# Kernel optimization log

Measured on AMD Instinct MI355X. Metric: run time of the kernel, lower is better.

The kernel has to match this reference:

```python
import jax, jax.numpy as jnp
import numpy as np

N_NODES = 100000
N_EDGES = 3200000
HID = 16


def _graph_conv(x, src, dst, w_rel, w_root, b_rel, num_nodes):
    # PyG GraphConv: out_i = lin_rel(sum_{j in N(i)} x_j) + lin_root(x_i)
    agg = jax.ops.segment_sum(x[src], dst, num_segments=num_nodes)  # [N, d_in]
    return agg @ w_rel + b_rel + x @ w_root


def setup_inputs() -> dict:
    key = jax.random.key(0)
    ks = jax.random.split(key, 8)
    x = jax.random.normal(ks[0], (N_NODES, 1), dtype=jnp.float32)
    edge_index = jax.random.randint(ks[1], (2, N_EDGES), 0, N_NODES, dtype=jnp.int64)
    s = 1.0 / np.sqrt(HID)
    return {
        "x": x,
        "edge_index": edge_index,
        "enc_w_rel": jax.random.uniform(ks[2], (1, HID), jnp.float32, -1.0, 1.0),
        "enc_w_root": jax.random.uniform(ks[3], (1, HID), jnp.float32, -1.0, 1.0),
        "enc_b": jnp.zeros((HID,), jnp.float32),
        "proc_w_rel": jax.random.uniform(ks[4], (HID, HID), jnp.float32, -s, s),
        "proc_w_root": jax.random.uniform(ks[5], (HID, HID), jnp.float32, -s, s),
        "proc_b": jnp.zeros((HID,), jnp.float32),
        "dec_w_rel": jax.random.uniform(ks[6], (HID, 1), jnp.float32, -s, s),
        "dec_w_root": jax.random.uniform(ks[7], (HID, 1), jnp.float32, -s, s),
        "dec_b": jnp.zeros((1,), jnp.float32),
    }


def reference(x, edge_index, enc_w_rel, enc_w_root, enc_b,
              proc_w_rel, proc_w_root, proc_b,
              dec_w_rel, dec_w_root, dec_b):
    num_nodes = x.shape[0]
    src, dst = edge_index[0], edge_index[1]
    z = _graph_conv(x, src, dst, enc_w_rel, enc_w_root, enc_b, num_nodes)
    z = jax.nn.relu(z)
    z = _graph_conv(z, src, dst, proc_w_rel, proc_w_root, proc_b, num_nodes)
    y = _graph_conv(z, src, dst, dec_w_rel, dec_w_root, dec_b, num_nodes)
    return jax.nn.relu(y)
```

## Files before the change

### kernel.cpp

```cpp
#include <hip/hip_runtime.h>
#include <hip/hip_bf16.h>

#define HID 16
#define SB_BITS 11
#define SBLK (1 << SB_BITS)
#define SUBS 128
#define NBMAX 64
#define GSTRIDE 16
#define PT_THREADS 512
#define PT_K 8
#define PT_EDGES (PT_THREADS * PT_K)
#define ROWP 65

__global__ void k_init(int* __restrict__ p, int n) {
    int i = blockIdx.x * blockDim.x + threadIdx.x;
    if (i < n) p[i] = 0;
}

__global__ void __launch_bounds__(PT_THREADS)
k_passA(const int* __restrict__ src, const int* __restrict__ dst,
        unsigned* __restrict__ bucketsA, int* __restrict__ gcurA,
        int E, int nb, int capA) {
    __shared__ int cnt[NBMAX];
    __shared__ int pos[NBMAX];
    __shared__ int gbase[NBMAX];
    __shared__ unsigned reorder[PT_EDGES];
    __shared__ unsigned char bbk[PT_EDGES];
    int tb = blockIdx.x * PT_EDGES;
    int nE = min(PT_EDGES, E - tb);
    if (threadIdx.x < nb) cnt[threadIdx.x] = 0;
    __syncthreads();
    int kk[PT_K]; int rk[PT_K]; unsigned pk[PT_K];
    int ebase = tb + threadIdx.x * PT_K;
    if (ebase + PT_K <= E) {
        uint4 s0 = *(const uint4*)(src + ebase);
        uint4 s1 = *(const uint4*)(src + ebase + 4);
        uint4 d0 = *(const uint4*)(dst + ebase);
        uint4 d1 = *(const uint4*)(dst + ebase + 4);
        int ss[PT_K] = {(int)s0.x,(int)s0.y,(int)s0.z,(int)s0.w,
                        (int)s1.x,(int)s1.y,(int)s1.z,(int)s1.w};
        int dd[PT_K] = {(int)d0.x,(int)d0.y,(int)d0.z,(int)d0.w,
                        (int)d1.x,(int)d1.y,(int)d1.z,(int)d1.w};
#pragma unroll
        for (int k = 0; k < PT_K; k++) {
            int b = dd[k] >> SB_BITS;
            kk[k] = b;
            pk[k] = ((unsigned)(dd[k] & (SBLK - 1)) << 17) | (unsigned)ss[k];
            rk[k] = atomicAdd(&cnt[b], 1);
        }
    } else {
#pragma unroll
        for (int k = 0; k < PT_K; k++) {
            int e = ebase + k;
            if (e < E) {
                int s = src[e], d = dst[e];
                int b = d >> SB_BITS;
                kk[k] = b;
                pk[k] = ((unsigned)(d & (SBLK - 1)) << 17) | (unsigned)s;
                rk[k] = atomicAdd(&cnt[b], 1);
            } else kk[k] = -1;
        }
    }
    __syncthreads();
    if (threadIdx.x == 0) {
        int acc = 0;
        for (int b = 0; b < nb; b++) { pos[b] = acc; acc += cnt[b]; }
    }
    __syncthreads();
    if (threadIdx.x < nb && cnt[threadIdx.x] > 0)
        gbase[threadIdx.x] = atomicAdd(&gcurA[threadIdx.x * GSTRIDE], cnt[threadIdx.x]);
    __syncthreads();
#pragma unroll
    for (int k = 0; k < PT_K; k++) {
        if (kk[k] >= 0) {
            int idx = pos[kk[k]] + rk[k];
            reorder[idx] = pk[k];
            bbk[idx] = (unsigned char)kk[k];
        }
    }
    __syncthreads();
    for (int idx = threadIdx.x; idx < nE; idx += PT_THREADS) {
        int b = bbk[idx];
        int g = gbase[b] + (idx - pos[b]);
        if (g < capA) bucketsA[(size_t)b * capA + g] = reorder[idx];
    }
}

__global__ void __launch_bounds__(PT_THREADS)
k_passB(const unsigned* __restrict__ bucketsA, const int* __restrict__ gcurA,
        unsigned* __restrict__ bucketsB, int* __restrict__ gcurB,
        int capA, int capSub, int tilesB) {
    int j = blockIdx.x / tilesB;
    int tile = blockIdx.x - j * tilesB;
    int cnt_j = min(gcurA[j * GSTRIDE], capA);
    int tb = tile * PT_EDGES;
    if (tb >= cnt_j) return;
    int nE = min(PT_EDGES, cnt_j - tb);
    __shared__ int cnt[SUBS];
    __shared__ int pos[SUBS];
    __shared__ int gb[SUBS];
    __shared__ unsigned reorder[PT_EDGES];
    if (threadIdx.x < SUBS) cnt[threadIdx.x] = 0;
    __syncthreads();
    const unsigned* in = bucketsA + (size_t)j * capA + tb;
    int kk[PT_K]; int rk[PT_K]; unsigned pk[PT_K];
    int ebase = threadIdx.x * PT_K;
    if (ebase + PT_K <= nE) {
        uint4 p0 = *(const uint4*)(in + ebase);
        uint4 p1 = *(const uint4*)(in + ebase + 4);
        unsigned pp[PT_K] = {p0.x, p0.y, p0.z, p0.w, p1.x, p1.y, p1.z, p1.w};
#pragma unroll
        for (int k = 0; k < PT_K; k++) {
            int s = (int)(pp[k] >> 21);
            kk[k] = s;
            pk[k] = pp[k];
            rk[k] = atomicAdd(&cnt[s], 1);
        }
    } else {
#pragma unroll
        for (int k = 0; k < PT_K; k++) {
            int e = ebase + k;
            if (e < nE) {
                unsigned p = in[e];
                int s = (int)(p >> 21);
                kk[k] = s;
                pk[k] = p;
                rk[k] = atomicAdd(&cnt[s], 1);
            } else kk[k] = -1;
        }
    }
    __syncthreads();
    if (threadIdx.x == 0) {
        int acc = 0;
        for (int s = 0; s < SUBS; s++) { pos[s] = acc; acc += cnt[s]; }
    }
    __syncthreads();
    if (threadIdx.x < SUBS && cnt[threadIdx.x] > 0)
        gb[threadIdx.x] = atomicAdd(&gcurB[j * SUBS + threadIdx.x], cnt[threadIdx.x]);
    __syncthreads();
#pragma unroll
    for (int k = 0; k < PT_K; k++) {
        if (kk[k] >= 0) {
            int idx = pos[kk[k]] + rk[k];
            reorder[idx] = pk[k];
        }
    }
    __syncthreads();
    for (int idx = threadIdx.x; idx < nE; idx += PT_THREADS) {
        unsigned p = reorder[idx];
        int s = (int)(p >> 21);
        unsigned outp = ((p & 0x1FFFFu) << 4) | ((p >> 17) & 15u);
        int g = gb[s] + (idx - pos[s]);
        if (g < capSub) bucketsB[(size_t)(j * SUBS + s) * capSub + g] = outp;
    }
}

__global__ void __launch_bounds__(256)
k_agg1enc(const unsigned* __restrict__ bk2, const int* __restrict__ gcurB,
          const float* __restrict__ x,
          const float* __restrict__ ewrel, const float* __restrict__ ewroot,
          const float* __restrict__ eb,
          const float* __restrict__ pwrel, const float* __restrict__ pwroot,
          const float* __restrict__ dwrel, const float* __restrict__ dwroot,
          float* __restrict__ SAB, float* __restrict__ G1, float* __restrict__ G2,
          int capSub, int N) {
    __shared__ float P[4 * 16 * ROWP];
    __shared__ float su1[HID], su2[HID], sv1[HID], sv2[HID];
    __shared__ float swr[HID], swo[HID], sbb[HID];
    int t = threadIdx.x;
    if (t < 64) {
        int k = t & 15, w = t >> 4;
        const float* M  = (w < 2) ? pwrel : pwroot;
        const float* vv = ((w & 1) == 0) ? dwrel : dwroot;
        float acc = 0.f;
        for (int h = 0; h < HID; h++) acc += M[k * HID + h] * vv[h];
        if (w == 0) su1[k] = acc;
        else if (w == 1) su2[k] = acc;
        else if (w == 2) sv1[k] = acc;
        else sv2[k] = acc;
    }
    if (t < HID) { swr[t] = ewrel[t]; swo[t] = ewroot[t]; sbb[t] = eb[t]; }
    int wv = t >> 6, lane = t & 63;
    int q = blockIdx.x * 4 + wv;
    float* p = P + wv * 16 * ROWP;
#pragma unroll
    for (int d = 0; d < 16; d++) p[d * ROWP + lane] = 0.f;
    __syncthreads();
    int cnt = min(gcurB[q], capSub);
    const unsigned* bk = bk2 + (size_t)q * capSub;
    int base = 0;
    for (; base + 256 <= cnt; base += 256) {
        uint4 p4 = *(const uint4*)(bk + base + (lane << 2));
        float v0 = x[p4.x >> 4], v1 = x[p4.y >> 4], v2 = x[p4.z >> 4], v3 = x[p4.w >> 4];
        p[(int)(p4.x & 15) * ROWP + lane] += v0;
        p[(int)(p4.y & 15) * ROWP + lane] += v1;
        p[(int)(p4.z & 15) * ROWP + lane] += v2;
        p[(int)(p4.w & 15) * ROWP + lane] += v3;
    }
    for (int e = base + lane; e < cnt; e += 64) {
        unsigned pk = bk[e];
        p[(int)(pk & 15) * ROWP + lane] += x[pk >> 4];
    }
    __builtin_amdgcn_wave_barrier();
    int d = lane & 15, c0 = (lane >> 4) * 16;
    float s = 0.f;
#pragma unroll
    for (int k = 0; k < 16; k++) s += p[d * ROWP + c0 + k];
    s += __shfl_xor(s, 16);
    s += __shfl_xor(s, 32);
    if (lane < 16) {
        int n = q * 16 + lane;
        if (n < N) {
            float a1 = s, xi = x[n];
            float sa = 0.f, sb = 0.f, g1 = 0.f, g2 = 0.f;
#pragma unroll
            for (int h = 0; h < HID; h++) {
                float z = fmaxf(fmaf(a1, swr[h], fmaf(xi, swo[h], sbb[h])), 0.f);
                sa = fmaf(z, su1[h], sa);
                sb = fmaf(z, su2[h], sb);
                g1 = fmaf(z, sv1[h], g1);
                g2 = fmaf(z, sv2[h], g2);
            }
            ((float2*)SAB)[n] = make_float2(sa, sb);
            G1[n] = g1; G2[n] = g2;
        }
    }
}

__global__ void __launch_bounds__(256)
k_agg2mid(const unsigned* __restrict__ bk2, const int* __restrict__ gcurB,
          const float* __restrict__ SAB,
          const float* __restrict__ G1, const float* __restrict__ G2,
          const float* __restrict__ pb, const float* __restrict__ dwrel,
          const float* __restrict__ dwroot, const float* __restrict__ db,
          float* __restrict__ BETA, float* __restrict__ R,
          int capSub, int N) {
    __shared__ float2 P2[4 * 16 * ROWP];
    __shared__ float sc1, sc2, sbd;
    int t = threadIdx.x;
    if (t == 0) {
        float c1 = 0.f, c2 = 0.f;
        for (int h = 0; h < HID; h++) { c1 += pb[h] * dwrel[h]; c2 += pb[h] * dwroot[h]; }
        sc1 = c1; sc2 = c2; sbd = db[0];
    }
    int wv = t >> 6, lane = t & 63;
    int q = blockIdx.x * 4 + wv;
    float2* pw = P2 + wv * 16 * ROWP;
#pragma unroll
    for (int d = 0; d < 16; d++) pw[d * ROWP + lane] = make_float2(0.f, 0.f);
    __syncthreads();
    int cnt = min(gcurB[q], capSub);
    const unsigned* bk = bk2 + (size_t)q * capSub;
    const float2* v2 = (const float2*)SAB;
    int base = 0;
    for (; base + 256 <= cnt; base += 256) {
        uint4 p4 = *(const uint4*)(bk + base + (lane << 2));
        float2 v0 = v2[p4.x >> 4], v1 = v2[p4.y >> 4];
        float2 w2 = v2[p4.z >> 4], w3 = v2[p4.w >> 4];
        float2* s0 = &pw[(int)(p4.x & 15) * ROWP + lane];
        s0->x += v0.x; s0->y += v0.y;
        float2* s1 = &pw[(int)(p4.y & 15) * ROWP + lane];
        s1->x += v1.x; s1->y += v1.y;
        float2* s2 = &pw[(int)(p4.z & 15) * ROWP + lane];
        s2->x += w2.x; s2->y += w2.y;
        float2* s3 = &pw[(int)(p4.w & 15) * ROWP + lane];
        s3->x += w3.x; s3->y += w3.y;
    }
    for (int e = base + lane; e < cnt; e += 64) {
        unsigned pk = bk[e];
        float2 v = v2[pk >> 4];
        float2* s = &pw[(int)(pk & 15) * ROWP + lane];
        s->x += v.x; s->y += v.y;
    }
    __builtin_amdgcn_wave_barrier();
    int d = lane & 15, c0 = (lane >> 4) * 16;
    float sa = 0.f, sb = 0.f;
#pragma unroll
    for (int k = 0; k < 16; k++) {
        float2 v = pw[d * ROWP + c0 + k];
        sa += v.x; sb += v.y;
    }
    sa += __shfl_xor(sa, 16); sa += __shfl_xor(sa, 32);
    sb += __shfl_xor(sb, 16); sb += __shfl_xor(sb, 32);
    if (lane < 16) {
        int n = q * 16 + lane;
        if (n < N) {
            BETA[n] = sa + G1[n] + sc1;
            R[n]    = sb + G2[n] + sc2 + sbd;
        }
    }
}

__global__ void __launch_bounds__(256)
k_agg1f(const unsigned* __restrict__ bk2, const int* __restrict__ gcurB,
        const float* __restrict__ val, const float* __restrict__ R,
        float* __restrict__ out, int capSub, int N) {
    __shared__ float P[4 * 16 * ROWP];
    int wv = threadIdx.x >> 6, lane = threadIdx.x & 63;
    int q = blockIdx.x * 4 + wv;
    float* p = P + wv * 16 * ROWP;
#pragma unroll
    for (int d = 0; d < 16; d++) p[d * ROWP + lane] = 0.f;
    int cnt = min(gcurB[q], capSub);
    const unsigned* bk = bk2 + (size_t)q * capSub;
    int base = 0;
    for (; base + 256 <= cnt; base += 256) {
        uint4 p4 = *(const uint4*)(bk + base + (lane << 2));
        float v0 = val[p4.x >> 4], v1 = val[p4.y >> 4];
        float v2 = val[p4.z >> 4], v3 = val[p4.w >> 4];
        p[(int)(p4.x & 15) * ROWP + lane] += v0;
        p[(int)(p4.y & 15) * ROWP + lane] += v1;
        p[(int)(p4.z & 15) * ROWP + lane] += v2;
        p[(int)(p4.w & 15) * ROWP + lane] += v3;
    }
    for (int e = base + lane; e < cnt; e += 64) {
        unsigned pk = bk[e];
        p[(int)(pk & 15) * ROWP + lane] += val[pk >> 4];
    }
    __builtin_amdgcn_wave_barrier();
    int d = lane & 15, c0 = (lane >> 4) * 16;
    float s = 0.f;
#pragma unroll
    for (int k = 0; k < 16; k++) s += p[d * ROWP + c0 + k];
    s += __shfl_xor(s, 16);
    s += __shfl_xor(s, 32);
    if (lane < 16) {
        int n = q * 16 + lane;
        if (n < N) out[n] = fmaxf(s + R[n], 0.f);
    }
}

extern "C" void kernel_launch(void* const* d_in, const int* in_sizes, int n_in,
                              void* d_out, int out_size, void* d_ws, size_t ws_size,
                              hipStream_t stream) {
    const float* x      = (const float*)d_in[0];
    const int*   ei     = (const int*)d_in[1];
    const float* ewrel  = (const float*)d_in[2];
    const float* ewroot = (const float*)d_in[3];
    const float* eb     = (const float*)d_in[4];
    const float* pwrel  = (const float*)d_in[5];
    const float* pwroot = (const float*)d_in[6];
    const float* pb     = (const float*)d_in[7];
    const float* dwrel  = (const float*)d_in[8];
    const float* dwroot = (const float*)d_in[9];
    const float* db     = (const float*)d_in[10];
    float* out = (float*)d_out;

    const int N = in_sizes[0];
    const int E = in_sizes[1] / 2;
    const int* src = ei;
    const int* dst = ei + E;

    const int nb = (N + SBLK - 1) >> SB_BITS;
    int capA = ((E / nb + 2048) + PT_EDGES - 1) & ~(PT_EDGES - 1);
    const int tilesB = capA / PT_EDGES;
    const int nq = nb * SUBS;
    int capSub = ((E / nq + 226) + 3) & ~3;

    size_t off = 0;
    int* gcurA = (int*)d_ws;                    off += NBMAX * GSTRIDE;
    int* gcurB = (int*)d_ws + off;              off += nq;
    const int zeroWords = (int)off;
    off = (off + 255) & ~(size_t)255;
    unsigned* bucketsA = (unsigned*)d_ws + off; off += (size_t)nb * capA;
    unsigned* bucketsB = (unsigned*)d_ws + off; off += (size_t)nq * capSub;
    float* SAB  = (float*)d_ws + off;           off += (size_t)2 * N;
    float* G1   = (float*)d_ws + off;           off += N;
    float* G2   = (float*)d_ws + off;           off += N;
    float* BETA = (float*)d_ws + off;           off += N;
    float* R    = (float*)d_ws + off;           off += N;

    const int ntilesA = (E + PT_EDGES - 1) / PT_EDGES;
    const int aggBlocks = nq / 4;

    hipLaunchKernelGGL(k_init, dim3((zeroWords + 255) / 256), dim3(256), 0, stream,
                       gcurA, zeroWords);
    hipLaunchKernelGGL(k_passA, dim3(ntilesA), dim3(PT_THREADS), 0, stream,
                       src, dst, bucketsA, gcurA, E, nb, capA);
    hipLaunchKernelGGL(k_passB, dim3(nb * tilesB), dim3(PT_THREADS), 0, stream,
                       bucketsA, gcurA, bucketsB, gcurB, capA, capSub, tilesB);

    hipLaunchKernelGGL(k_agg1enc, dim3(aggBlocks), dim3(256), 0, stream,
                       bucketsB, gcurB, x, ewrel, ewroot, eb, pwrel, pwroot,
                       dwrel, dwroot, SAB, G1, G2, capSub, N);
    hipLaunchKernelGGL(k_agg2mid, dim3(aggBlocks), dim3(256), 0, stream,
                       bucketsB, gcurB, SAB, G1, G2, pb, dwrel, dwroot, db,
                       BETA, R, capSub, N);
    hipLaunchKernelGGL(k_agg1f, dim3(aggBlocks), dim3(256), 0, stream,
                       bucketsB, gcurB, BETA, R, out, capSub, N);
}
```

Measured before the change: 174.2 us.

## Drop second bucketing pass; aggregate via LDS float atomics per coarse bucket

Removes the passB sub-bucket sort and its bucketsB buffer. Each aggregation now reads the coarse passA buckets directly, accumulates into a 2048-entry shared-memory array with float atomics, and flushes to global per-node accumulators with global atomics. Per-node epilogue math moves into separate elementwise kernels. This saves one full scatter of the edge list but adds LDS atomic contention, global atomics from many tiles per bucket, and extra kernel launches, and the result becomes order-nondeterministic.

```diff
diff --git a/kernel.cpp b/kernel.cpp
--- a/kernel.cpp
+++ b/kernel.cpp
@@ -1,16 +1,13 @@
 #include <hip/hip_runtime.h>
-#include <hip/hip_bf16.h>
 
 #define HID 16
 #define SB_BITS 11
 #define SBLK (1 << SB_BITS)
-#define SUBS 128
 #define NBMAX 64
 #define GSTRIDE 16
 #define PT_THREADS 512
 #define PT_K 8
 #define PT_EDGES (PT_THREADS * PT_K)
-#define ROWP 65
 
 __global__ void k_init(int* __restrict__ p, int n) {
     int i = blockIdx.x * blockDim.x + threadIdx.x;
@@ -87,84 +84,111 @@
 }
 
 __global__ void __launch_bounds__(PT_THREADS)
-k_passB(const unsigned* __restrict__ bucketsA, const int* __restrict__ gcurA,
-        unsigned* __restrict__ bucketsB, int* __restrict__ gcurB,
-        int capA, int capSub, int tilesB) {
-    int j = blockIdx.x / tilesB;
-    int tile = blockIdx.x - j * tilesB;
+k_aggA1(const unsigned* __restrict__ bucketsA, const int* __restrict__ gcurA,
+        const float* __restrict__ val, float* __restrict__ AGG,
+        int capA, int tilesA, int N) {
+    int j = blockIdx.x / tilesA;
+    int tile = blockIdx.x - j * tilesA;
     int cnt_j = min(gcurA[j * GSTRIDE], capA);
     int tb = tile * PT_EDGES;
     if (tb >= cnt_j) return;
     int nE = min(PT_EDGES, cnt_j - tb);
-    __shared__ int cnt[SUBS];
-    __shared__ int pos[SUBS];
-    __shared__ int gb[SUBS];
-    __shared__ unsigned reorder[PT_EDGES];
-    if (threadIdx.x < SUBS) cnt[threadIdx.x] = 0;
+    __shared__ float acc[SBLK];
+    for (int i = threadIdx.x; i < SBLK; i += PT_THREADS) acc[i] = 0.f;
     __syncthreads();
     const unsigned* in = bucketsA + (size_t)j * capA + tb;
-    int kk[PT_K]; int rk[PT_K]; unsigned pk[PT_K];
     int ebase = threadIdx.x * PT_K;
     if (ebase + PT_K <= nE) {
         uint4 p0 = *(const uint4*)(in + ebase);
         uint4 p1 = *(const uint4*)(in + ebase + 4);
         unsigned pp[PT_K] = {p0.x, p0.y, p0.z, p0.w, p1.x, p1.y, p1.z, p1.w};
-#pragma unroll
-        for (int k = 0; k < PT_K; k++) {
-            int s = (int)(pp[k] >> 21);
-            kk[k] = s;
-            pk[k] = pp[k];
-            rk[k] = atomicAdd(&cnt[s], 1);
-        }
+        float v[PT_K];
+#pragma unroll
+        for (int k = 0; k < PT_K; k++) v[k] = val[pp[k] & 0x1FFFFu];
+#pragma unroll
+        for (int k = 0; k < PT_K; k++) atomicAdd(&acc[pp[k] >> 17], v[k]);
     } else {
 #pragma unroll
         for (int k = 0; k < PT_K; k++) {
             int e = ebase + k;
             if (e < nE) {
                 unsigned p = in[e];
-                int s = (int)(p >> 21);
-                kk[k] = s;
-                pk[k] = p;
-                rk[k] = atomicAdd(&cnt[s], 1);
-            } else kk[k] = -1;
-        }
-    }
-    __syncthreads();
-    if (threadIdx.x == 0) {
-        int acc = 0;
-        for (int s = 0; s < SUBS; s++) { pos[s] = acc; acc += cnt[s]; }
-    }
-    __syncthreads();
-    if (threadIdx.x < SUBS && cnt[threadIdx.x] > 0)
-        gb[threadIdx.x] = atomicAdd(&gcurB[j * SUBS + threadIdx.x], cnt[threadIdx.x]);
-    __syncthreads();
-#pragma unroll
-    for (int k = 0; k < PT_K; k++) {
-        if (kk[k] >= 0) {
-            int idx = pos[kk[k]] + rk[k];
-            reorder[idx] = pk[k];
-        }
-    }
-    __syncthreads();
-    for (int idx = threadIdx.x; idx < nE; idx += PT_THREADS) {
-        unsigned p = reorder[idx];
-        int s = (int)(p >> 21);
-        unsigned outp = ((p & 0x1FFFFu) << 4) | ((p >> 17) & 15u);
-        int g = gb[s] + (idx - pos[s]);
-        if (g < capSub) bucketsB[(size_t)(j * SUBS + s) * capSub + g] = outp;
+                atomicAdd(&acc[p >> 17], val[p & 0x1FFFFu]);
+            }
+        }
+    }
+    __syncthreads();
+    int base_n = j << SB_BITS;
+    for (int i = threadIdx.x; i < SBLK; i += PT_THREADS) {
+        float v = acc[i];
+        int n = base_n + i;
+        if (n < N && v != 0.f) atomicAdd(&AGG[n], v);
+    }
+}
+
+__global__ void __launch_bounds__(PT_THREADS)
+k_aggA2(const unsigned* __restrict__ bucketsA, const int* __restrict__ gcurA,
+        const float* __restrict__ SAB, float* __restrict__ AGG2,
+        int capA, int tilesA, int N) {
+    int j = blockIdx.x / tilesA;
+    int tile = blockIdx.x - j * tilesA;
+    int cnt_j = min(gcurA[j * GSTRIDE], capA);
+    int tb = tile * PT_EDGES;
+    if (tb >= cnt_j) return;
+    int nE = min(PT_EDGES, cnt_j - tb);
+    __shared__ float accx[SBLK];
+    __shared__ float accy[SBLK];
+    for (int i = threadIdx.x; i < SBLK; i += PT_THREADS) { accx[i] = 0.f; accy[i] = 0.f; }
+    __syncthreads();
+    const unsigned* in = bucketsA + (size_t)j * capA + tb;
+    const float2* v2 = (const float2*)SAB;
+    int ebase = threadIdx.x * PT_K;
+    if (ebase + PT_K <= nE) {
+        uint4 p0 = *(const uint4*)(in + ebase);
+        uint4 p1 = *(const uint4*)(in + ebase + 4);
+        unsigned pp[PT_K] = {p0.x, p0.y, p0.z, p0.w, p1.x, p1.y, p1.z, p1.w};
+        float2 v[PT_K];
+#pragma unroll
+        for (int k = 0; k < PT_K; k++) v[k] = v2[pp[k] & 0x1FFFFu];
+#pragma unroll
+        for (int k = 0; k < PT_K; k++) {
+            int d = (int)(pp[k] >> 17);
+            atomicAdd(&accx[d], v[k].x);
+            atomicAdd(&accy[d], v[k].y);
+        }
+    } else {
+#pragma unroll
+        for (int k = 0; k < PT_K; k++) {
+            int e = ebase + k;
+            if (e < nE) {
+                unsigned p = in[e];
+                float2 v = v2[p & 0x1FFFFu];
+                int d = (int)(p >> 17);
+                atomicAdd(&accx[d], v.x);
+                atomicAdd(&accy[d], v.y);
+            }
+        }
+    }
+    __syncthreads();
+    int base_n = j << SB_BITS;
+    for (int i = threadIdx.x; i < SBLK; i += PT_THREADS) {
+        float vx = accx[i], vy = accy[i];
+        int n = base_n + i;
+        if (n < N && (vx != 0.f || vy != 0.f)) {
+            atomicAdd(&AGG2[2 * n],     vx);
+            atomicAdd(&AGG2[2 * n + 1], vy);
+        }
     }
 }
 
 __global__ void __launch_bounds__(256)
-k_agg1enc(const unsigned* __restrict__ bk2, const int* __restrict__ gcurB,
-          const float* __restrict__ x,
-          const float* __restrict__ ewrel, const float* __restrict__ ewroot,
-          const float* __restrict__ eb,
-          const float* __restrict__ pwrel, const float* __restrict__ pwroot,
-          const float* __restrict__ dwrel, const float* __restrict__ dwroot,
-          float* __restrict__ SAB, float* __restrict__ G1, float* __restrict__ G2,
-          int capSub, int N) {
-    __shared__ float P[4 * 16 * ROWP];
+k_enc(const float* __restrict__ AGG1, const float* __restrict__ x,
+      const float* __restrict__ ewrel, const float* __restrict__ ewroot,
+      const float* __restrict__ eb,
+      const float* __restrict__ pwrel, const float* __restrict__ pwroot,
+      const float* __restrict__ dwrel, const float* __restrict__ dwroot,
+      float* __restrict__ SAB, float* __restrict__ G1, float* __restrict__ G2,
+      int N) {
     __shared__ float su1[HID], su2[HID], sv1[HID], sv2[HID];
     __shared__ float swr[HID], swo[HID], sbb[HID];
     int t = threadIdx.x;
@@ -180,154 +204,50 @@
         else sv2[k] = acc;
     }
     if (t < HID) { swr[t] = ewrel[t]; swo[t] = ewroot[t]; sbb[t] = eb[t]; }
-    int wv = t >> 6, lane = t & 63;
-    int q = blockIdx.x * 4 + wv;
-    float* p = P + wv * 16 * ROWP;
-#pragma unroll
-    for (int d = 0; d < 16; d++) p[d * ROWP + lane] = 0.f;
-    __syncthreads();
-    int cnt = min(gcurB[q], capSub);
-    const unsigned* bk = bk2 + (size_t)q * capSub;
-    int base = 0;
-    for (; base + 256 <= cnt; base += 256) {
-        uint4 p4 = *(const uint4*)(bk + base + (lane << 2));
-        float v0 = x[p4.x >> 4], v1 = x[p4.y >> 4], v2 = x[p4.z >> 4], v3 = x[p4.w >> 4];
-        p[(int)(p4.x & 15) * ROWP + lane] += v0;
-        p[(int)(p4.y & 15) * ROWP + lane] += v1;
-        p[(int)(p4.z & 15) * ROWP + lane] += v2;
-        p[(int)(p4.w & 15) * ROWP + lane] += v3;
-    }
-    for (int e = base + lane; e < cnt; e += 64) {
-        unsigned pk = bk[e];
-        p[(int)(pk & 15) * ROWP + lane] += x[pk >> 4];
-    }
-    __builtin_amdgcn_wave_barrier();
-    int d = lane & 15, c0 = (lane >> 4) * 16;
-    float s = 0.f;
-#pragma unroll
-    for (int k = 0; k < 16; k++) s += p[d * ROWP + c0 + k];
-    s += __shfl_xor(s, 16);
-    s += __shfl_xor(s, 32);
-    if (lane < 16) {
-        int n = q * 16 + lane;
-        if (n < N) {
-            float a1 = s, xi = x[n];
-            float sa = 0.f, sb = 0.f, g1 = 0.f, g2 = 0.f;
-#pragma unroll
-            for (int h = 0; h < HID; h++) {
-                float z = fmaxf(fmaf(a1, swr[h], fmaf(xi, swo[h], sbb[h])), 0.f);
-                sa = fmaf(z, su1[h], sa);
-                sb = fmaf(z, su2[h], sb);
-                g1 = fmaf(z, sv1[h], g1);
-                g2 = fmaf(z, sv2[h], g2);
-            }
-            ((float2*)SAB)[n] = make_float2(sa, sb);
-            G1[n] = g1; G2[n] = g2;
-        }
+    __syncthreads();
+    int n = blockIdx.x * 256 + t;
+    if (n < N) {
+        float a1 = AGG1[n], xi = x[n];
+        float sa = 0.f, sb = 0.f, g1 = 0.f, g2 = 0.f;
+#pragma unroll
+        for (int h = 0; h < HID; h++) {
+            float z = fmaxf(fmaf(a1, swr[h], fmaf(xi, swo[h], sbb[h])), 0.f);
+            sa = fmaf(z, su1[h], sa);
+            sb = fmaf(z, su2[h], sb);
+            g1 = fmaf(z, sv1[h], g1);
+            g2 = fmaf(z, sv2[h], g2);
+        }
+        ((float2*)SAB)[n] = make_float2(sa, sb);
+        G1[n] = g1; G2[n] = g2;
     }
 }
 
 __global__ void __launch_bounds__(256)
-k_agg2mid(const unsigned* __restrict__ bk2, const int* __restrict__ gcurB,
-          const float* __restrict__ SAB,
-          const float* __restrict__ G1, const float* __restrict__ G2,
-          const float* __restrict__ pb, const float* __restrict__ dwrel,
-          const float* __restrict__ dwroot, const float* __restrict__ db,
-          float* __restrict__ BETA, float* __restrict__ R,
-          int capSub, int N) {
-    __shared__ float2 P2[4 * 16 * ROWP];
+k_mid(const float* __restrict__ AGG2, const float* __restrict__ G1,
+      const float* __restrict__ G2, const float* __restrict__ pb,
+      const float* __restrict__ dwrel, const float* __restrict__ dwroot,
+      const float* __restrict__ db,
+      float* __restrict__ BETA, float* __restrict__ R, int N) {
     __shared__ float sc1, sc2, sbd;
-    int t = threadIdx.x;
-    if (t == 0) {
+    if (threadIdx.x == 0) {
         float c1 = 0.f, c2 = 0.f;
         for (int h = 0; h < HID; h++) { c1 += pb[h] * dwrel[h]; c2 += pb[h] * dwroot[h]; }
         sc1 = c1; sc2 = c2; sbd = db[0];
     }
-    int wv = t >> 6, lane = t & 63;
-    int q = blockIdx.x * 4 + wv;
-    float2* pw = P2 + wv * 16 * ROWP;
-#pragma unroll
-    for (int d = 0; d < 16; d++) pw[d * ROWP + lane] = make_float2(0.f, 0.f);
-    __syncthreads();
-    int cnt = min(gcurB[q], capSub);
-    const unsigned* bk = bk2 + (size_t)q * capSub;
-    const float2* v2 = (const float2*)SAB;
-    int base = 0;
-    for (; base + 256 <= cnt; base += 256) {
-        uint4 p4 = *(const uint4*)(bk + base + (lane << 2));
-        float2 v0 = v2[p4.x >> 4], v1 = v2[p4.y >> 4];
-        float2 w2 = v2[p4.z >> 4], w3 = v2[p4.w >> 4];
-        float2* s0 = &pw[(int)(p4.x & 15) * ROWP + lane];
-        s0->x += v0.x; s0->y += v0.y;
-        float2* s1 = &pw[(int)(p4.y & 15) * ROWP + lane];
-        s1->x += v1.x; s1->y += v1.y;
-        float2* s2 = &pw[(int)(p4.z & 15) * ROWP + lane];
-        s2->x += w2.x; s2->y += w2.y;
-        float2* s3 = &pw[(int)(p4.w & 15) * ROWP + lane];
-        s3->x += w3.x; s3->y += w3.y;
-    }
-    for (int e = base + lane; e < cnt; e += 64) {
-        unsigned pk = bk[e];
-        float2 v = v2[pk >> 4];
-        float2* s = &pw[(int)(pk & 15) * ROWP + lane];
-        s->x += v.x; s->y += v.y;
-    }
-    __builtin_amdgcn_wave_barrier();
-    int d = lane & 15, c0 = (lane >> 4) * 16;
-    float sa = 0.f, sb = 0.f;
-#pragma unroll
-    for (int k = 0; k < 16; k++) {
-        float2 v = pw[d * ROWP + c0 + k];
-        sa += v.x; sb += v.y;
-    }
-    sa += __shfl_xor(sa, 16); sa += __shfl_xor(sa, 32);
-    sb += __shfl_xor(sb, 16); sb += __shfl_xor(sb, 32);
-    if (lane < 16) {
-        int n = q * 16 + lane;
-        if (n < N) {
-            BETA[n] = sa + G1[n] + sc1;
-            R[n]    = sb + G2[n] + sc2 + sbd;
-        }
+    __syncthreads();
+    int n = blockIdx.x * 256 + threadIdx.x;
+    if (n < N) {
+        float2 a = ((const float2*)AGG2)[n];
+        BETA[n] = a.x + G1[n] + sc1;
+        R[n]    = a.y + G2[n] + sc2 + sbd;
     }
 }
 
 __global__ void __launch_bounds__(256)
-k_agg1f(const unsigned* __restrict__ bk2, const int* __restrict__ gcurB,
-        const float* __restrict__ val, const float* __restrict__ R,
-        float* __restrict__ out, int capSub, int N) {
-    __shared__ float P[4 * 16 * ROWP];
-    int wv = threadIdx.x >> 6, lane = threadIdx.x & 63;
-    int q = blockIdx.x * 4 + wv;
-    float* p = P + wv * 16 * ROWP;
-#pragma unroll
-    for (int d = 0; d < 16; d++) p[d * ROWP + lane] = 0.f;
-    int cnt = min(gcurB[q], capSub);
-    const unsigned* bk = bk2 + (size_t)q * capSub;
-    int base = 0;
-    for (; base + 256 <= cnt; base += 256) {
-        uint4 p4 = *(const uint4*)(bk + base + (lane << 2));
-        float v0 = val[p4.x >> 4], v1 = val[p4.y >> 4];
-        float v2 = val[p4.z >> 4], v3 = val[p4.w >> 4];
-        p[(int)(p4.x & 15) * ROWP + lane] += v0;
-        p[(int)(p4.y & 15) * ROWP + lane] += v1;
-        p[(int)(p4.z & 15) * ROWP + lane] += v2;
-        p[(int)(p4.w & 15) * ROWP + lane] += v3;
-    }
-    for (int e = base + lane; e < cnt; e += 64) {
-        unsigned pk = bk[e];
-        p[(int)(pk & 15) * ROWP + lane] += val[pk >> 4];
-    }
-    __builtin_amdgcn_wave_barrier();
-    int d = lane & 15, c0 = (lane >> 4) * 16;
-    float s = 0.f;
-#pragma unroll
-    for (int k = 0; k < 16; k++) s += p[d * ROWP + c0 + k];
-    s += __shfl_xor(s, 16);
-    s += __shfl_xor(s, 32);
-    if (lane < 16) {
-        int n = q * 16 + lane;
-        if (n < N) out[n] = fmaxf(s + R[n], 0.f);
-    }
+k_final(const float* __restrict__ AGG3, const float* __restrict__ R,
+        float* __restrict__ out, int N) {
+    int n = blockIdx.x * 256 + threadIdx.x;
+    if (n < N) out[n] = fmaxf(AGG3[n] + R[n], 0.f);
 }
 
 extern "C" void kernel_launch(void* const* d_in, const int* in_sizes, int n_in,
@@ -353,17 +273,16 @@
 
     const int nb = (N + SBLK - 1) >> SB_BITS;
     int capA = ((E / nb + 2048) + PT_EDGES - 1) & ~(PT_EDGES - 1);
-    const int tilesB = capA / PT_EDGES;
-    const int nq = nb * SUBS;
-    int capSub = ((E / nq + 226) + 3) & ~3;
+    const int tilesA = capA / PT_EDGES;
 
     size_t off = 0;
     int* gcurA = (int*)d_ws;                    off += NBMAX * GSTRIDE;
-    int* gcurB = (int*)d_ws + off;              off += nq;
+    float* AGG1 = (float*)d_ws + off;           off += N;
+    float* AGG2 = (float*)d_ws + off;           off += (size_t)2 * N;
+    float* AGG3 = (float*)d_ws + off;           off += N;
     const int zeroWords = (int)off;
     off = (off + 255) & ~(size_t)255;
     unsigned* bucketsA = (unsigned*)d_ws + off; off += (size_t)nb * capA;
-    unsigned* bucketsB = (unsigned*)d_ws + off; off += (size_t)nq * capSub;
     float* SAB  = (float*)d_ws + off;           off += (size_t)2 * N;
     float* G1   = (float*)d_ws + off;           off += N;
     float* G2   = (float*)d_ws + off;           off += N;
@@ -371,21 +290,27 @@
     float* R    = (float*)d_ws + off;           off += N;
 
     const int ntilesA = (E + PT_EDGES - 1) / PT_EDGES;
-    const int aggBlocks = nq / 4;
+    const int aggGrid = nb * tilesA;
+    const int nodeBlocks = (N + 255) / 256;
 
     hipLaunchKernelGGL(k_init, dim3((zeroWords + 255) / 256), dim3(256), 0, stream,
                        gcurA, zeroWords);
     hipLaunchKernelGGL(k_passA, dim3(ntilesA), dim3(PT_THREADS), 0, stream,
                        src, dst, bucketsA, gcurA, E, nb, capA);
-    hipLaunchKernelGGL(k_passB, dim3(nb * tilesB), dim3(PT_THREADS), 0, stream,
-                       bucketsA, gcurA, bucketsB, gcurB, capA, capSub, tilesB);
-
-    hipLaunchKernelGGL(k_agg1enc, dim3(aggBlocks), dim3(256), 0, stream,
-                       bucketsB, gcurB, x, ewrel, ewroot, eb, pwrel, pwroot,
-                       dwrel, dwroot, SAB, G1, G2, capSub, N);
-    hipLaunchKernelGGL(k_agg2mid, dim3(aggBlocks), dim3(256), 0, stream,
-                       bucketsB, gcurB, SAB, G1, G2, pb, dwrel, dwroot, db,
-                       BETA, R, capSub, N);
-    hipLaunchKernelGGL(k_agg1f, dim3(aggBlocks), dim3(256), 0, stream,
-                       bucketsB, gcurB, BETA, R, out, capSub, N);
-}
+
+    hipLaunchKernelGGL(k_aggA1, dim3(aggGrid), dim3(PT_THREADS), 0, stream,
+                       bucketsA, gcurA, x, AGG1, capA, tilesA, N);
+    hipLaunchKernelGGL(k_enc, dim3(nodeBlocks), dim3(256), 0, stream,
+                       AGG1, x, ewrel, ewroot, eb, pwrel, pwroot,
+                       dwrel, dwroot, SAB, G1, G2, N);
+
+    hipLaunchKernelGGL(k_aggA2, dim3(aggGrid), dim3(PT_THREADS), 0, stream,
+                       bucketsA, gcurA, SAB, AGG2, capA, tilesA, N);
+    hipLaunchKernelGGL(k_mid, dim3(nodeBlocks), dim3(256), 0, stream,
+                       AGG2, G1, G2, pb, dwrel, dwroot, db, BETA, R, N);
+
+    hipLaunchKernelGGL(k_aggA1, dim3(aggGrid), dim3(PT_THREADS), 0, stream,
+                       bucketsA, gcurA, BETA, AGG3, capA, tilesA, N);
+    hipLaunchKernelGGL(k_final, dim3(nodeBlocks), dim3(256), 0, stream,
+                       AGG3, R, out, N);
+}
```

After: 211.7 us. +21.6%, slower.

## Fuse first-layer aggregation into bucket pass B and deepen gather batching

Applied to the files above, without the earlier changes.

The first scalar aggregation moves into the second bucketing pass. Each tile accumulates x[src] into a 2048-slot LDS array with shared atomics and writes a per-tile partial slab, and a new lightweight per-node encoder kernel sums the slabs. This removes one full pass over the sub-buckets and its gathers. The other aggregation kernels now gather 8 edges per lane per iteration instead of 4 to expose more memory-level parallelism. The cost is extra LDS atomics and partial-slab traffic in pass B, and a changed floating-point summation order.

```diff
diff --git a/kernel.cpp b/kernel.cpp
--- a/kernel.cpp
+++ b/kernel.cpp
@@ -1,5 +1,4 @@
 #include <hip/hip_runtime.h>
-#include <hip/hip_bf16.h>
 
 #define HID 16
 #define SB_BITS 11
@@ -87,11 +86,13 @@
 }
 
 __global__ void __launch_bounds__(PT_THREADS)
-k_passB(const unsigned* __restrict__ bucketsA, const int* __restrict__ gcurA,
-        unsigned* __restrict__ bucketsB, int* __restrict__ gcurB,
-        int capA, int capSub, int tilesB) {
-    int j = blockIdx.x / tilesB;
-    int tile = blockIdx.x - j * tilesB;
+k_passBagg1(const unsigned* __restrict__ bucketsA, const int* __restrict__ gcurA,
+            const float* __restrict__ x,
+            unsigned* __restrict__ bucketsB, int* __restrict__ gcurB,
+            float* __restrict__ PART1,
+            int capA, int capSub, int tilesA) {
+    int j = blockIdx.x / tilesA;
+    int tile = blockIdx.x - j * tilesA;
     int cnt_j = min(gcurA[j * GSTRIDE], capA);
     int tb = tile * PT_EDGES;
     if (tb >= cnt_j) return;
@@ -100,7 +101,9 @@
     __shared__ int pos[SUBS];
     __shared__ int gb[SUBS];
     __shared__ unsigned reorder[PT_EDGES];
+    __shared__ float acc[SBLK];
     if (threadIdx.x < SUBS) cnt[threadIdx.x] = 0;
+    for (int i = threadIdx.x; i < SBLK; i += PT_THREADS) acc[i] = 0.f;
     __syncthreads();
     const unsigned* in = bucketsA + (size_t)j * capA + tb;
     int kk[PT_K]; int rk[PT_K]; unsigned pk[PT_K];
@@ -109,12 +112,16 @@
         uint4 p0 = *(const uint4*)(in + ebase);
         uint4 p1 = *(const uint4*)(in + ebase + 4);
         unsigned pp[PT_K] = {p0.x, p0.y, p0.z, p0.w, p1.x, p1.y, p1.z, p1.w};
+        float xv[PT_K];
+#pragma unroll
+        for (int k = 0; k < PT_K; k++) xv[k] = x[pp[k] & 0x1FFFFu];
 #pragma unroll
         for (int k = 0; k < PT_K; k++) {
             int s = (int)(pp[k] >> 21);
             kk[k] = s;
             pk[k] = pp[k];
             rk[k] = atomicAdd(&cnt[s], 1);
+            atomicAdd(&acc[pp[k] >> 17], xv[k]);
         }
     } else {
 #pragma unroll
@@ -126,13 +133,14 @@
                 kk[k] = s;
                 pk[k] = p;
                 rk[k] = atomicAdd(&cnt[s], 1);
+                atomicAdd(&acc[p >> 17], x[p & 0x1FFFFu]);
             } else kk[k] = -1;
         }
     }
     __syncthreads();
     if (threadIdx.x == 0) {
-        int acc = 0;
-        for (int s = 0; s < SUBS; s++) { pos[s] = acc; acc += cnt[s]; }
+        int a = 0;
+        for (int s = 0; s < SUBS; s++) { pos[s] = a; a += cnt[s]; }
     }
     __syncthreads();
     if (threadIdx.x < SUBS && cnt[threadIdx.x] > 0)
@@ -153,18 +161,19 @@
         int g = gb[s] + (idx - pos[s]);
         if (g < capSub) bucketsB[(size_t)(j * SUBS + s) * capSub + g] = outp;
     }
+    float* slab = PART1 + (size_t)(j * tilesA + tile) * SBLK;
+    for (int i = threadIdx.x; i < SBLK; i += PT_THREADS) slab[i] = acc[i];
 }
 
 __global__ void __launch_bounds__(256)
-k_agg1enc(const unsigned* __restrict__ bk2, const int* __restrict__ gcurB,
-          const float* __restrict__ x,
-          const float* __restrict__ ewrel, const float* __restrict__ ewroot,
-          const float* __restrict__ eb,
-          const float* __restrict__ pwrel, const float* __restrict__ pwroot,
-          const float* __restrict__ dwrel, const float* __restrict__ dwroot,
-          float* __restrict__ SAB, float* __restrict__ G1, float* __restrict__ G2,
-          int capSub, int N) {
-    __shared__ float P[4 * 16 * ROWP];
+k_enc(const float* __restrict__ PART1, const int* __restrict__ gcurA,
+      const float* __restrict__ x,
+      const float* __restrict__ ewrel, const float* __restrict__ ewroot,
+      const float* __restrict__ eb,
+      const float* __restrict__ pwrel, const float* __restrict__ pwroot,
+      const float* __restrict__ dwrel, const float* __restrict__ dwroot,
+      float* __restrict__ SAB, float* __restrict__ G1, float* __restrict__ G2,
+      int capA, int tilesA, int N) {
     __shared__ float su1[HID], su2[HID], sv1[HID], sv2[HID];
     __shared__ float swr[HID], swo[HID], sbb[HID];
     int t = threadIdx.x;
@@ -180,50 +189,27 @@
         else sv2[k] = acc;
     }
     if (t < HID) { swr[t] = ewrel[t]; swo[t] = ewroot[t]; sbb[t] = eb[t]; }
-    int wv = t >> 6, lane = t & 63;
-    int q = blockIdx.x * 4 + wv;
-    float* p = P + wv * 16 * ROWP;
-#pragma unroll
-    for (int d = 0; d < 16; d++) p[d * ROWP + lane] = 0.f;
-    __syncthreads();
-    int cnt = min(gcurB[q], capSub);
-    const unsigned* bk = bk2 + (size_t)q * capSub;
-    int base = 0;
-    for (; base + 256 <= cnt; base += 256) {
-        uint4 p4 = *(const uint4*)(bk + base + (lane << 2));
-        float v0 = x[p4.x >> 4], v1 = x[p4.y >> 4], v2 = x[p4.z >> 4], v3 = x[p4.w >> 4];
-        p[(int)(p4.x & 15) * ROWP + lane] += v0;
-        p[(int)(p4.y & 15) * ROWP + lane] += v1;
-        p[(int)(p4.z & 15) * ROWP + lane] += v2;
-        p[(int)(p4.w & 15) * ROWP + lane] += v3;
-    }
-    for (int e = base + lane; e < cnt; e += 64) {
-        unsigned pk = bk[e];
-        p[(int)(pk & 15) * ROWP + lane] += x[pk >> 4];
-    }
-    __builtin_amdgcn_wave_barrier();
-    int d = lane & 15, c0 = (lane >> 4) * 16;
-    float s = 0.f;
-#pragma unroll
-    for (int k = 0; k < 16; k++) s += p[d * ROWP + c0 + k];
-    s += __shfl_xor(s, 16);
-    s += __shfl_xor(s, 32);
-    if (lane < 16) {
-        int n = q * 16 + lane;
-        if (n < N) {
-            float a1 = s, xi = x[n];
-            float sa = 0.f, sb = 0.f, g1 = 0.f, g2 = 0.f;
-#pragma unroll
-            for (int h = 0; h < HID; h++) {
-                float z = fmaxf(fmaf(a1, swr[h], fmaf(xi, swo[h], sbb[h])), 0.f);
-                sa = fmaf(z, su1[h], sa);
-                sb = fmaf(z, su2[h], sb);
-                g1 = fmaf(z, sv1[h], g1);
-                g2 = fmaf(z, sv2[h], g2);
-            }
-            ((float2*)SAB)[n] = make_float2(sa, sb);
-            G1[n] = g1; G2[n] = g2;
-        }
+    __syncthreads();
+    int n = blockIdx.x * 256 + t;
+    if (n < N) {
+        int j = n >> SB_BITS, slot = n & (SBLK - 1);
+        int cnt_j = min(gcurA[j * GSTRIDE], capA);
+        int nt = min(tilesA, (cnt_j + PT_EDGES - 1) / PT_EDGES);
+        float a1 = 0.f;
+        const float* pl = PART1 + (size_t)j * tilesA * SBLK + slot;
+        for (int tt = 0; tt < nt; tt++) a1 += pl[tt * SBLK];
+        float xi = x[n];
+        float sa = 0.f, sb = 0.f, g1 = 0.f, g2 = 0.f;
+#pragma unroll
+        for (int h = 0; h < HID; h++) {
+            float z = fmaxf(fmaf(a1, swr[h], fmaf(xi, swo[h], sbb[h])), 0.f);
+            sa = fmaf(z, su1[h], sa);
+            sb = fmaf(z, su2[h], sb);
+            g1 = fmaf(z, sv1[h], g1);
+            g2 = fmaf(z, sv2[h], g2);
+        }
+        ((float2*)SAB)[n] = make_float2(sa, sb);
+        G1[n] = g1; G2[n] = g2;
     }
 }
 
@@ -253,18 +239,19 @@
     const unsigned* bk = bk2 + (size_t)q * capSub;
     const float2* v2 = (const float2*)SAB;
     int base = 0;
-    for (; base + 256 <= cnt; base += 256) {
-        uint4 p4 = *(const uint4*)(bk + base + (lane << 2));
-        float2 v0 = v2[p4.x >> 4], v1 = v2[p4.y >> 4];
-        float2 w2 = v2[p4.z >> 4], w3 = v2[p4.w >> 4];
-        float2* s0 = &pw[(int)(p4.x & 15) * ROWP + lane];
-        s0->x += v0.x; s0->y += v0.y;
-        float2* s1 = &pw[(int)(p4.y & 15) * ROWP + lane];
-        s1->x += v1.x; s1->y += v1.y;
-        float2* s2 = &pw[(int)(p4.z & 15) * ROWP + lane];
-        s2->x += w2.x; s2->y += w2.y;
-        float2* s3 = &pw[(int)(p4.w & 15) * ROWP + lane];
-        s3->x += w3.x; s3->y += w3.y;
+    for (; base + 512 <= cnt; base += 512) {
+        const unsigned* bp = bk + base + (lane << 3);
+        uint4 a4 = *(const uint4*)bp;
+        uint4 b4 = *(const uint4*)(bp + 4);
+        unsigned pp[8] = {a4.x, a4.y, a4.z, a4.w, b4.x, b4.y, b4.z, b4.w};
+        float2 vv[8];
+#pragma unroll
+        for (int k = 0; k < 8; k++) vv[k] = v2[pp[k] >> 4];
+#pragma unroll
+        for (int k = 0; k < 8; k++) {
+            float2* s = &pw[(int)(pp[k] & 15) * ROWP + lane];
+            s->x += vv[k].x; s->y += vv[k].y;
+        }
     }
     for (int e = base + lane; e < cnt; e += 64) {
         unsigned pk = bk[e];
@@ -304,14 +291,17 @@
     int cnt = min(gcurB[q], capSub);
     const unsigned* bk = bk2 + (size_t)q * capSub;
     int base = 0;
-    for (; base + 256 <= cnt; base += 256) {
-        uint4 p4 = *(const uint4*)(bk + base + (lane << 2));
-        float v0 = val[p4.x >> 4], v1 = val[p4.y >> 4];
-        float v2 = val[p4.z >> 4], v3 = val[p4.w >> 4];
-        p[(int)(p4.x & 15) * ROWP + lane] += v0;
-        p[(int)(p4.y & 15) * ROWP + lane] += v1;
-        p[(int)(p4.z & 15) * ROWP + lane] += v2;
-        p[(int)(p4.w & 15) * ROWP + lane] += v3;
+    for (; base + 512 <= cnt; base += 512) {
+        const unsigned* bp = bk + base + (lane << 3);
+        uint4 a4 = *(const uint4*)bp;
+        uint4 b4 = *(const uint4*)(bp + 4);
+        unsigned pp[8] = {a4.x, a4.y, a4.z, a4.w, b4.x, b4.y, b4.z, b4.w};
+        float vv[8];
+#pragma unroll
+        for (int k = 0; k < 8; k++) vv[k] = val[pp[k] >> 4];
+#pragma unroll
+        for (int k = 0; k < 8; k++)
+            p[(int)(pp[k] & 15) * ROWP + lane] += vv[k];
     }
     for (int e = base + lane; e < cnt; e += 64) {
         unsigned pk = bk[e];
@@ -353,7 +343,7 @@
 
     const int nb = (N + SBLK - 1) >> SB_BITS;
     int capA = ((E / nb + 2048) + PT_EDGES - 1) & ~(PT_EDGES - 1);
-    const int tilesB = capA / PT_EDGES;
+    const int tilesA = capA / PT_EDGES;
     const int nq = nb * SUBS;
     int capSub = ((E / nq + 226) + 3) & ~3;
 
@@ -364,6 +354,7 @@
     off = (off + 255) & ~(size_t)255;
     unsigned* bucketsA = (unsigned*)d_ws + off; off += (size_t)nb * capA;
     unsigned* bucketsB = (unsigned*)d_ws + off; off += (size_t)nq * capSub;
+    float* PART1 = (float*)d_ws + off;          off += (size_t)nb * tilesA * SBLK;
     float* SAB  = (float*)d_ws + off;           off += (size_t)2 * N;
     float* G1   = (float*)d_ws + off;           off += N;
     float* G2   = (float*)d_ws + off;           off += N;
@@ -371,18 +362,23 @@
     float* R    = (float*)d_ws + off;           off += N;
 
     const int ntilesA = (E + PT_EDGES - 1) / PT_EDGES;
+    const int passBGrid = nb * tilesA;
     const int aggBlocks = nq / 4;
+    const int nodeBlocks = (N + 255) / 256;
 
     hipLaunchKernelGGL(k_init, dim3((zeroWords + 255) / 256), dim3(256), 0, stream,
                        gcurA, zeroWords);
     hipLaunchKernelGGL(k_passA, dim3(ntilesA), dim3(PT_THREADS), 0, stream,
                        src, dst, bucketsA, gcurA, E, nb, capA);
-    hipLaunchKernelGGL(k_passB, dim3(nb * tilesB), dim3(PT_THREADS), 0, stream,
-                       bucketsA, gcurA, bucketsB, gcurB, capA, capSub, tilesB);
-
-    hipLaunchKernelGGL(k_agg1enc, dim3(aggBlocks), dim3(256), 0, stream,
-                       bucketsB, gcurB, x, ewrel, ewroot, eb, pwrel, pwroot,
-                       dwrel, dwroot, SAB, G1, G2, capSub, N);
+
+    hipLaunchKernelGGL(k_passBagg1, dim3(passBGrid), dim3(PT_THREADS), 0, stream,
+                       bucketsA, gcurA, x, bucketsB, gcurB, PART1,
+                       capA, capSub, tilesA);
+
+    hipLaunchKernelGGL(k_enc, dim3(nodeBlocks), dim3(256), 0, stream,
+                       PART1, gcurA, x, ewrel, ewroot, eb, pwrel, pwroot,
+                       dwrel, dwroot, SAB, G1, G2, capA, tilesA, N);
+
     hipLaunchKernelGGL(k_agg2mid, dim3(aggBlocks), dim3(256), 0, stream,
                        bucketsB, gcurB, SAB, G1, G2, pb, dwrel, dwroot, db,
                        BETA, R, capSub, N);
```

Result: slower. 188.5 us (+8.2%).

## Use wave-level match aggregation for bucket counters and widen gather unroll

Applied to the files above, without the earlier changes.

In both bucketing passes, the per-edge shared-memory atomicAdd is replaced by a ballot-based match. Lanes with the same bucket are grouped, one leader issues a single atomic with the group count, and the others derive their rank with a popcount. This targets LDS atomic contention on hot buckets, at the cost of 6-8 ballots per edge and extra shared scratch. The three aggregation kernels also process 8 edges per lane per iteration instead of 4, so more independent gathers are in flight.

```diff
diff --git a/kernel.cpp b/kernel.cpp
--- a/kernel.cpp
+++ b/kernel.cpp
@@ -1,5 +1,4 @@
 #include <hip/hip_runtime.h>
-#include <hip/hip_bf16.h>
 
 #define HID 16
 #define SB_BITS 11
@@ -24,12 +23,15 @@
     __shared__ int cnt[NBMAX];
     __shared__ int pos[NBMAX];
     __shared__ int gbase[NBMAX];
+    __shared__ int swb[8 * NBMAX];
     __shared__ unsigned reorder[PT_EDGES];
     __shared__ unsigned char bbk[PT_EDGES];
     int tb = blockIdx.x * PT_EDGES;
     int nE = min(PT_EDGES, E - tb);
     if (threadIdx.x < nb) cnt[threadIdx.x] = 0;
     __syncthreads();
+    int lane = threadIdx.x & 63, wv = threadIdx.x >> 6;
+    int ss[PT_K], dd[PT_K]; bool vld[PT_K];
     int kk[PT_K]; int rk[PT_K]; unsigned pk[PT_K];
     int ebase = tb + threadIdx.x * PT_K;
     if (ebase + PT_K <= E) {
@@ -37,29 +39,37 @@
         uint4 s1 = *(const uint4*)(src + ebase + 4);
         uint4 d0 = *(const uint4*)(dst + ebase);
         uint4 d1 = *(const uint4*)(dst + ebase + 4);
-        int ss[PT_K] = {(int)s0.x,(int)s0.y,(int)s0.z,(int)s0.w,
-                        (int)s1.x,(int)s1.y,(int)s1.z,(int)s1.w};
-        int dd[PT_K] = {(int)d0.x,(int)d0.y,(int)d0.z,(int)d0.w,
-                        (int)d1.x,(int)d1.y,(int)d1.z,(int)d1.w};
-#pragma unroll
-        for (int k = 0; k < PT_K; k++) {
-            int b = dd[k] >> SB_BITS;
-            kk[k] = b;
-            pk[k] = ((unsigned)(dd[k] & (SBLK - 1)) << 17) | (unsigned)ss[k];
-            rk[k] = atomicAdd(&cnt[b], 1);
-        }
+        ss[0]=(int)s0.x; ss[1]=(int)s0.y; ss[2]=(int)s0.z; ss[3]=(int)s0.w;
+        ss[4]=(int)s1.x; ss[5]=(int)s1.y; ss[6]=(int)s1.z; ss[7]=(int)s1.w;
+        dd[0]=(int)d0.x; dd[1]=(int)d0.y; dd[2]=(int)d0.z; dd[3]=(int)d0.w;
+        dd[4]=(int)d1.x; dd[5]=(int)d1.y; dd[6]=(int)d1.z; dd[7]=(int)d1.w;
+#pragma unroll
+        for (int k = 0; k < PT_K; k++) vld[k] = true;
     } else {
 #pragma unroll
         for (int k = 0; k < PT_K; k++) {
             int e = ebase + k;
-            if (e < E) {
-                int s = src[e], d = dst[e];
-                int b = d >> SB_BITS;
-                kk[k] = b;
-                pk[k] = ((unsigned)(d & (SBLK - 1)) << 17) | (unsigned)s;
-                rk[k] = atomicAdd(&cnt[b], 1);
-            } else kk[k] = -1;
-        }
+            vld[k] = (e < E);
+            ss[k] = vld[k] ? src[e] : 0;
+            dd[k] = vld[k] ? dst[e] : 0;
+        }
+    }
+#pragma unroll
+    for (int k = 0; k < PT_K; k++) {
+        int b = vld[k] ? (dd[k] >> SB_BITS) : 63;
+        kk[k] = vld[k] ? b : -1;
+        pk[k] = ((unsigned)(dd[k] & (SBLK - 1)) << 17) | (unsigned)ss[k];
+        unsigned long long mm = ~0ull;
+#pragma unroll
+        for (int p = 0; p < 6; p++) {
+            unsigned long long bal = __ballot((b >> p) & 1);
+            mm &= ((b >> p) & 1) ? bal : ~bal;
+        }
+        mm &= __builtin_amdgcn_read_exec();
+        int rank = __popcll(mm & ((1ull << lane) - 1ull));
+        if (rank == 0) swb[(wv << 6) + b] = atomicAdd(&cnt[b], __popcll(mm));
+        __builtin_amdgcn_wave_barrier();
+        rk[k] = swb[(wv << 6) + b] + rank;
     }
     __syncthreads();
     if (threadIdx.x == 0) {
@@ -96,38 +106,48 @@
     int tb = tile * PT_EDGES;
     if (tb >= cnt_j) return;
     int nE = min(PT_EDGES, cnt_j - tb);
-    __shared__ int cnt[SUBS];
+    __shared__ int cnt[136];
     __shared__ int pos[SUBS];
     __shared__ int gb[SUBS];
+    __shared__ int swb[8 * 136];
     __shared__ unsigned reorder[PT_EDGES];
-    if (threadIdx.x < SUBS) cnt[threadIdx.x] = 0;
-    __syncthreads();
+    for (int i = threadIdx.x; i < 136; i += PT_THREADS) cnt[i] = 0;
+    __syncthreads();
+    int lane = threadIdx.x & 63, wv = threadIdx.x >> 6;
     const unsigned* in = bucketsA + (size_t)j * capA + tb;
-    int kk[PT_K]; int rk[PT_K]; unsigned pk[PT_K];
+    unsigned pp[PT_K]; bool vld[PT_K];
+    int kk[PT_K]; int rk[PT_K];
     int ebase = threadIdx.x * PT_K;
     if (ebase + PT_K <= nE) {
         uint4 p0 = *(const uint4*)(in + ebase);
         uint4 p1 = *(const uint4*)(in + ebase + 4);
-        unsigned pp[PT_K] = {p0.x, p0.y, p0.z, p0.w, p1.x, p1.y, p1.z, p1.w};
-#pragma unroll
-        for (int k = 0; k < PT_K; k++) {
-            int s = (int)(pp[k] >> 21);
-            kk[k] = s;
-            pk[k] = pp[k];
-            rk[k] = atomicAdd(&cnt[s], 1);
-        }
+        pp[0]=p0.x; pp[1]=p0.y; pp[2]=p0.z; pp[3]=p0.w;
+        pp[4]=p1.x; pp[5]=p1.y; pp[6]=p1.z; pp[7]=p1.w;
+#pragma unroll
+        for (int k = 0; k < PT_K; k++) vld[k] = true;
     } else {
 #pragma unroll
         for (int k = 0; k < PT_K; k++) {
             int e = ebase + k;
-            if (e < nE) {
-                unsigned p = in[e];
-                int s = (int)(p >> 21);
-                kk[k] = s;
-                pk[k] = p;
-                rk[k] = atomicAdd(&cnt[s], 1);
-            } else kk[k] = -1;
-        }
+            vld[k] = (e < nE);
+            pp[k] = vld[k] ? in[e] : 0u;
+        }
+    }
+#pragma unroll
+    for (int k = 0; k < PT_K; k++) {
+        int b = vld[k] ? (int)(pp[k] >> 21) : 128;
+        kk[k] = vld[k] ? b : -1;
+        unsigned long long mm = ~0ull;
+#pragma unroll
+        for (int p = 0; p < 8; p++) {
+            unsigned long long bal = __ballot((b >> p) & 1);
+            mm &= ((b >> p) & 1) ? bal : ~bal;
+        }
+        mm &= __builtin_amdgcn_read_exec();
+        int rank = __popcll(mm & ((1ull << lane) - 1ull));
+        if (rank == 0) swb[wv * 136 + b] = atomicAdd(&cnt[b], __popcll(mm));
+        __builtin_amdgcn_wave_barrier();
+        rk[k] = swb[wv * 136 + b] + rank;
     }
     __syncthreads();
     if (threadIdx.x == 0) {
@@ -142,7 +162,7 @@
     for (int k = 0; k < PT_K; k++) {
         if (kk[k] >= 0) {
             int idx = pos[kk[k]] + rk[k];
-            reorder[idx] = pk[k];
+            reorder[idx] = pp[k];
         }
     }
     __syncthreads();
@@ -189,13 +209,17 @@
     int cnt = min(gcurB[q], capSub);
     const unsigned* bk = bk2 + (size_t)q * capSub;
     int base = 0;
-    for (; base + 256 <= cnt; base += 256) {
-        uint4 p4 = *(const uint4*)(bk + base + (lane << 2));
-        float v0 = x[p4.x >> 4], v1 = x[p4.y >> 4], v2 = x[p4.z >> 4], v3 = x[p4.w >> 4];
-        p[(int)(p4.x & 15) * ROWP + lane] += v0;
-        p[(int)(p4.y & 15) * ROWP + lane] += v1;
-        p[(int)(p4.z & 15) * ROWP + lane] += v2;
-        p[(int)(p4.w & 15) * ROWP + lane] += v3;
+    for (; base + 512 <= cnt; base += 512) {
+        const unsigned* bp = bk + base + (lane << 3);
+        uint4 a4 = *(const uint4*)bp;
+        uint4 b4 = *(const uint4*)(bp + 4);
+        unsigned pp[8] = {a4.x, a4.y, a4.z, a4.w, b4.x, b4.y, b4.z, b4.w};
+        float vv[8];
+#pragma unroll
+        for (int k = 0; k < 8; k++) vv[k] = x[pp[k] >> 4];
+#pragma unroll
+        for (int k = 0; k < 8; k++)
+            p[(int)(pp[k] & 15) * ROWP + lane] += vv[k];
     }
     for (int e = base + lane; e < cnt; e += 64) {
         unsigned pk = bk[e];
@@ -253,18 +277,19 @@
     const unsigned* bk = bk2 + (size_t)q * capSub;
     const float2* v2 = (const float2*)SAB;
     int base = 0;
-    for (; base + 256 <= cnt; base += 256) {
-        uint4 p4 = *(const uint4*)(bk + base + (lane << 2));
-        float2 v0 = v2[p4.x >> 4], v1 = v2[p4.y >> 4];
-        float2 w2 = v2[p4.z >> 4], w3 = v2[p4.w >> 4];
-        float2* s0 = &pw[(int)(p4.x & 15) * ROWP + lane];
-        s0->x += v0.x; s0->y += v0.y;
-        float2* s1 = &pw[(int)(p4.y & 15) * ROWP + lane];
-        s1->x += v1.x; s1->y += v1.y;
-        float2* s2 = &pw[(int)(p4.z & 15) * ROWP + lane];
-        s2->x += w2.x; s2->y += w2.y;
-        float2* s3 = &pw[(int)(p4.w & 15) * ROWP + lane];
-        s3->x += w3.x; s3->y += w3.y;
+    for (; base + 512 <= cnt; base += 512) {
+        const unsigned* bp = bk + base + (lane << 3);
+        uint4 a4 = *(const uint4*)bp;
+        uint4 b4 = *(const uint4*)(bp + 4);
+        unsigned pp[8] = {a4.x, a4.y, a4.z, a4.w, b4.x, b4.y, b4.z, b4.w};
+        float2 vv[8];
+#pragma unroll
+        for (int k = 0; k < 8; k++) vv[k] = v2[pp[k] >> 4];
+#pragma unroll
+        for (int k = 0; k < 8; k++) {
+            float2* s = &pw[(int)(pp[k] & 15) * ROWP + lane];
+            s->x += vv[k].x; s->y += vv[k].y;
+        }
     }
     for (int e = base + lane; e < cnt; e += 64) {
         unsigned pk = bk[e];
@@ -304,14 +329,17 @@
     int cnt = min(gcurB[q], capSub);
     const unsigned* bk = bk2 + (size_t)q * capSub;
     int base = 0;
-    for (; base + 256 <= cnt; base += 256) {
-        uint4 p4 = *(const uint4*)(bk + base + (lane << 2));
-        float v0 = val[p4.x >> 4], v1 = val[p4.y >> 4];
-        float v2 = val[p4.z >> 4], v3 = val[p4.w >> 4];
-        p[(int)(p4.x & 15) * ROWP + lane] += v0;
-        p[(int)(p4.y & 15) * ROWP + lane] += v1;
-        p[(int)(p4.z & 15) * ROWP + lane] += v2;
-        p[(int)(p4.w & 15) * ROWP + lane] += v3;
+    for (; base + 512 <= cnt; base += 512) {
+        const unsigned* bp = bk + base + (lane << 3);
+        uint4 a4 = *(const uint4*)bp;
+        uint4 b4 = *(const uint4*)(bp + 4);
+        unsigned pp[8] = {a4.x, a4.y, a4.z, a4.w, b4.x, b4.y, b4.z, b4.w};
+        float vv[8];
+#pragma unroll
+        for (int k = 0; k < 8; k++) vv[k] = val[pp[k] >> 4];
+#pragma unroll
+        for (int k = 0; k < 8; k++)
+            p[(int)(pp[k] & 15) * ROWP + lane] += vv[k];
     }
     for (int e = base + lane; e < cnt; e += 64) {
         unsigned pk = bk[e];
```

After: 180.8 us. 3.8% more time.
